# Kernel optimization log

Hardware: AMD Instinct MI355X
Metric: run time of the kernel (lower is better)

## Reference

```python
import jax, jax.numpy as jnp
import numpy as np

EMBED_DIM = 1024
N_HEADS = 16
HEAD_DIM = EMBED_DIM // N_HEADS


def setup_inputs() -> dict:
    key = jax.random.key(0)
    k1, k2, k3 = jax.random.split(key, 3)
    B, T, C = 2, 2048, EMBED_DIM
    x = jax.random.normal(k1, (B, T, C), dtype=jnp.float32)
    # nn.Linear-style init scale
    s = 1.0 / np.sqrt(C)
    Wqkv = jax.random.normal(k2, (C, 3 * C), dtype=jnp.float32) * s
    bqkv = jnp.zeros((3 * C,), dtype=jnp.float32)
    Wout = jax.random.normal(k3, (C, C), dtype=jnp.float32) * s
    bout = jnp.zeros((C,), dtype=jnp.float32)
    return {"x": x, "Wqkv": Wqkv, "bqkv": bqkv, "Wout": Wout, "bout": bout}


def reference(x, Wqkv, bqkv, Wout, bout):
    B, T, C = x.shape
    H, D = N_HEADS, HEAD_DIM
    qkv = x @ Wqkv + bqkv  # [B,T,3C]
    q, k, v = jnp.split(qkv, 3, axis=-1)
    # [B,T,C] -> [B,H,T,D]
    q = q.reshape(B, T, H, D).transpose(0, 2, 1, 3)
    k = k.reshape(B, T, H, D).transpose(0, 2, 1, 3)
    v = v.reshape(B, T, H, D).transpose(0, 2, 1, 3)
    scale = 1.0 / np.sqrt(D)
    scores = jnp.einsum("bhqd,bhkd->bhqk", q, k) * scale  # [B,H,T,T]
    causal = jnp.tril(jnp.ones((T, T), dtype=bool))  # True where allowed
    scores = jnp.where(causal, scores, jnp.finfo(scores.dtype).min)
    attn = jax.nn.softmax(scores, axis=-1)
    out = jnp.einsum("bhqk,bhkd->bhqd", attn, v)  # [B,H,T,D]
    out = out.transpose(0, 2, 1, 3).reshape(B, T, C)
    return out @ Wout + bout
```

## Files before the change

kernel.cpp:

```cpp
#include <hip/hip_runtime.h>
#include <hip/hip_bf16.h>
#include <stdint.h>

#define EMBED 1024
#define NH 16
#define HD 64
#define BATCH 2
#define SEQ 2048
#define MTOK (BATCH*SEQ)

using bf8 = __attribute__((ext_vector_type(8))) short;
using f4  = __attribute__((ext_vector_type(4))) float;
using f16v = __attribute__((ext_vector_type(16))) float;
using u16x4 = __attribute__((ext_vector_type(4))) unsigned short;

union U4 { uint32_t u[4]; bf8 v; };

__device__ __forceinline__ uint32_t pk_bf16(float a, float b) {
  __hip_bfloat162 h = __float22bfloat162_rn(float2{a, b});
  union { __hip_bfloat162 h; uint32_t u; } c; c.h = h; return c.u;
}
__device__ __forceinline__ unsigned short bfbits(float f) {
  __hip_bfloat16 h = __float2bfloat16(f);
  union { __hip_bfloat16 h; unsigned short u; } c; c.h = h; return c.u;
}
__device__ __forceinline__ float bf2f(unsigned short u) {
  union { uint32_t u; float f; } c; c.u = (uint32_t)u << 16; return c.f;
}
__device__ __forceinline__ float fexp2(float x) {
#if __has_builtin(__builtin_amdgcn_exp2f)
  return __builtin_amdgcn_exp2f(x);
#else
  return exp2f(x);
#endif
}
__device__ __forceinline__ float frcp(float x) {
#if __has_builtin(__builtin_amdgcn_rcpf)
  return __builtin_amdgcn_rcpf(x);
#else
  return 1.f / x;
#endif
}

__device__ __forceinline__ void gl2lds16(const void* g, void* l) {
  __builtin_amdgcn_global_load_lds(
      (const __attribute__((address_space(1))) void*)g,
      (__attribute__((address_space(3))) void*)l, 16, 0, 0);
}

__global__ __launch_bounds__(256) void prep(const float* __restrict__ x,
                                            unsigned short* __restrict__ xb,
                                            const float* __restrict__ Wqkv,
                                            unsigned short* __restrict__ wqkvT,
                                            const float* __restrict__ Wout,
                                            unsigned short* __restrict__ woutT) {
  __shared__ float tl[64][65];
  int blk = blockIdx.x;
  if (blk < 4096) {
    int i = (blk * 256 + threadIdx.x) * 4;
    float4 v = *(const float4*)(x + i);
    uint2 o;
    o.x = pk_bf16(v.x, v.y);
    o.y = pk_bf16(v.z, v.w);
    *(uint2*)(xb + i) = o;
    return;
  }
  const float* W; unsigned short* Wt; int K, N, bx, by;
  if (blk < 4096 + 768) {
    int j = blk - 4096; W = Wqkv; Wt = wqkvT; K = 1024; N = 3072;
    bx = j % 48; by = j / 48;
  } else {
    int j = blk - 4096 - 768; W = Wout; Wt = woutT; K = 1024; N = 1024;
    bx = j % 16; by = j / 16;
  }
  int k0 = by * 64, n0 = bx * 64;
  int tr = threadIdx.x >> 6, tc = threadIdx.x & 63;
#pragma unroll
  for (int i = 0; i < 16; i++) {
    int r = tr + i * 4;
    tl[r][tc] = W[(size_t)(k0 + r) * N + n0 + tc];
  }
  __syncthreads();
#pragma unroll
  for (int i = 0; i < 16; i++) {
    int r = tr + i * 4;
    Wt[(size_t)(n0 + r) * K + k0 + tc] = bfbits(tl[tc][r]);
  }
}

template<int MODE>
__global__ __launch_bounds__(256) void gemm_bt(const unsigned short* __restrict__ A,
                                               const unsigned short* __restrict__ Bt,
                                               const float* __restrict__ bias,
                                               unsigned short* __restrict__ Oq,
                                               unsigned short* __restrict__ Ov,
                                               float* __restrict__ Of,
                                               int M, int N, int K) {
  const int tid = threadIdx.x;
  const int w = tid >> 6, lane = tid & 63;
  const int m0 = blockIdx.y * 128, n0 = blockIdx.x * 64;

  __shared__ char smem[49152];
  f4 acc[2][4] = {};

  auto STAGE = [&](int buf, int kk) {
    int k0 = kk * 64;
#pragma unroll
    for (int i = 0; i < 4; i++) {
      int c = i * 4 + w;
      int row = c * 8 + (lane >> 3);
      int col = ((lane & 7) * 8) ^ ((row & 7) << 3);
      gl2lds16(A + (size_t)(m0 + row) * K + k0 + col, smem + buf * 16384 + c * 1024);
    }
#pragma unroll
    for (int i = 0; i < 2; i++) {
      int c = i * 4 + w;
      int row = c * 8 + (lane >> 3);
      int col = ((lane & 7) * 8) ^ ((row & 7) << 3);
      gl2lds16(Bt + (size_t)(n0 + row) * K + k0 + col, smem + 32768 + buf * 8192 + c * 1024);
    }
  };

  const int nk = K / 64;
  STAGE(0, 0);
  STAGE(1, 1);

  for (int kk = 0; kk < nk; kk++) {
    if (kk + 1 < nk) {
      asm volatile("s_waitcnt vmcnt(6)" ::: "memory");
    } else {
      asm volatile("s_waitcnt vmcnt(0)" ::: "memory");
    }
    __builtin_amdgcn_s_barrier();

    const char* Al = smem + (kk & 1) * 16384;
    const char* Bl = smem + 32768 + (kk & 1) * 8192;
    __builtin_amdgcn_s_setprio(1);
#pragma unroll
    for (int ks = 0; ks < 2; ks++) {
      bf8 af[2], bfr[4];
#pragma unroll
      for (int mt = 0; mt < 2; mt++) {
        int rr = w * 32 + mt * 16 + (lane & 15);
        af[mt] = *(const bf8*)(Al + rr * 128 + ((ks * 64 + (lane >> 4) * 16) ^ ((rr & 7) << 4)));
      }
#pragma unroll
      for (int nt = 0; nt < 4; nt++) {
        int rr = nt * 16 + (lane & 15);
        bfr[nt] = *(const bf8*)(Bl + rr * 128 + ((ks * 64 + (lane >> 4) * 16) ^ ((rr & 7) << 4)));
      }
#pragma unroll
      for (int mt = 0; mt < 2; mt++)
#pragma unroll
        for (int nt = 0; nt < 4; nt++)
          acc[mt][nt] = __builtin_amdgcn_mfma_f32_16x16x32_bf16(af[mt], bfr[nt], acc[mt][nt], 0, 0, 0);
    }
    __builtin_amdgcn_s_setprio(0);

    __builtin_amdgcn_s_barrier();
    if (kk + 2 < nk) STAGE(kk & 1, kk + 2);
  }

  if (MODE == 0) {
    const int region = n0 >> 10;
    if (region < 2) {
      float sc = (region == 0) ? 0.180336880f : 1.0f;
#pragma unroll
      for (int nt = 0; nt < 4; nt++) {
        int n = n0 + nt * 16 + (lane & 15);
        float bv = bias[n];
        int c = n & 1023, h = c >> 6, d = c & 63;
#pragma unroll
        for (int mt = 0; mt < 2; mt++) {
#pragma unroll
          for (int r = 0; r < 4; r++) {
            int m = m0 + w * 32 + mt * 16 + (lane >> 4) * 4 + r;
            int b = m >> 11, t = m & 2047;
            size_t off = ((((size_t)region * 2 + b) * 16 + h) * 2048 + t) * 64 + d;
            Oq[off] = bfbits((acc[mt][nt][r] + bv) * sc);
          }
        }
      }
    } else {
#pragma unroll
      for (int nt = 0; nt < 4; nt++) {
        int n = n0 + nt * 16 + (lane & 15);
        float bv = bias[n];
        int c = n & 1023, h = c >> 6, d = c & 63;
#pragma unroll
        for (int mt = 0; mt < 2; mt++) {
          int m = m0 + w * 32 + mt * 16 + (lane >> 4) * 4;
          int b = m >> 11, t = m & 2047;
          size_t off = (((size_t)b * 16 + h) * 64 + d) * 2048 + t;
          u16x4 pk4;
#pragma unroll
          for (int r = 0; r < 4; r++) pk4[r] = bfbits(acc[mt][nt][r] + bv);
          *(u16x4*)(Ov + off) = pk4;
        }
      }
    }
  } else {
#pragma unroll
    for (int mt = 0; mt < 2; mt++) {
#pragma unroll
      for (int r = 0; r < 4; r++) {
        int m = m0 + w * 32 + mt * 16 + (lane >> 4) * 4 + r;
#pragma unroll
        for (int nt = 0; nt < 4; nt++) {
          int n = n0 + nt * 16 + (lane & 15);
          Of[(size_t)m * N + n] = acc[mt][nt][r] + bias[n];
        }
      }
    }
  }
}

__global__ __launch_bounds__(256) void attn12(const unsigned short* __restrict__ Qb,
                                              const unsigned short* __restrict__ Kb,
                                              const unsigned short* __restrict__ Vtb,
                                              unsigned short* __restrict__ Ob,
                                              unsigned short* __restrict__ partO,
                                              float* __restrict__ Lbuf) {
  static const signed char QTs[32] = {15,15,14,14,13,13,12,12,11,11,10,10,9,8,7,6,5,15,4,9,14,3,8,13,2,7,12,1,6,11,0,5};
  static const signed char TSs[32] = {0,11,0,11,0,11,0,11,0,11,0,11,0,0,0,0,0,22,0,11,22,0,11,22,0,11,22,0,11,22,0,11};
  static const signed char PS[32]  = {0,1,2,3,4,5,6,7,8,9,10,11,12,13,14,15,16,17,-1,18,19,-1,20,21,-1,22,23,-1,24,25,-1,26};
  const int idx = blockIdx.x;
  const int s = idx >> 5, bh = idx & 31;
  const int qt = QTs[s], ts = TSs[s];
  const int ntot = 2 * qt + 2;
  const int te = min(ts + 11, ntot);
  const int slot = PS[s];

  const int tid = threadIdx.x;
  const int w = tid >> 6, lane = tid & 63;
  const int hi = lane >> 5, q32 = lane & 31;

  __shared__ char smem[49152];

  const unsigned short* Qg  = Qb  + (size_t)bh * SEQ * HD;
  const unsigned short* Kg  = Kb  + (size_t)bh * SEQ * HD;
  const unsigned short* Vtg = Vtb + (size_t)bh * SEQ * HD;

  const int qbw  = qt * 128 + w * 32;
  const int qrow = qbw + q32;

  bf8 qf[4];
#pragma unroll
  for (int kc = 0; kc < 4; kc++)
    qf[kc] = *(const bf8*)(Qg + (size_t)qrow * HD + kc * 16 + hi * 8);

  f16v acc0 = {}, acc1 = {};
  float lr = 0.f;

  auto STAGE = [&](int buf, int t) {
    int kv0 = t * 64;
#pragma unroll
    for (int i = 0; i < 2; i++) {
      int c = i * 4 + w;
      int row = c * 8 + (lane >> 3);
      int col = ((lane & 7) * 8) ^ ((row & 7) << 3);
      gl2lds16(Kg + (size_t)(kv0 + row) * HD + col,    smem + buf * 8192 + c * 1024);
      gl2lds16(Vtg + (size_t)row * SEQ + kv0 + col,    smem + 24576 + buf * 8192 + c * 1024);
    }
  };

  const int nt_loc = te - ts;
  STAGE(0, ts);
  if (nt_loc > 1) STAGE(1, ts + 1);

  for (int tl = 0; tl < nt_loc; tl++) {
    const int t = ts + tl;
    const int kv0 = t * 64;

    if (tl + 1 < nt_loc) {
      asm volatile("s_waitcnt vmcnt(4)" ::: "memory");
    } else {
      asm volatile("s_waitcnt vmcnt(0)" ::: "memory");
    }
    __builtin_amdgcn_s_barrier();
    if (tl + 2 < nt_loc) STAGE((tl + 2) % 3, t + 2);

    if (kv0 <= qbw + 31) {
      const char* kl = smem + (tl % 3) * 8192;
      const char* vl = smem + 24576 + (tl % 3) * 8192;
      const bool hi_vis = (kv0 + 32 <= qbw + 31);

      f16v s0 = {}, s1 = {};
      __builtin_amdgcn_s_setprio(1);
#pragma unroll
      for (int kc = 0; kc < 4; kc++) {
        int r0 = q32;
        bf8 k0 = *(const bf8*)(kl + r0 * 128 + ((kc * 32 + hi * 16) ^ ((r0 & 7) << 4)));
        s0 = __builtin_amdgcn_mfma_f32_32x32x16_bf16(k0, qf[kc], s0, 0, 0, 0);
      }
      if (hi_vis) {
#pragma unroll
        for (int kc = 0; kc < 4; kc++) {
          int r1 = 32 + q32;
          bf8 k1 = *(const bf8*)(kl + r1 * 128 + ((kc * 32 + hi * 16) ^ ((r1 & 7) << 4)));
          s1 = __builtin_amdgcn_mfma_f32_32x32x16_bf16(k1, qf[kc], s1, 0, 0, 0);
        }
      }
      __builtin_amdgcn_s_setprio(0);

      if (kv0 + 63 > qbw) {
#pragma unroll
        for (int r = 0; r < 16; r++) {
          int key = kv0 + (r & 3) + 8 * (r >> 2) + 4 * hi;
          if (key > qrow)      s0[r] = -1e30f;
          if (key + 32 > qrow) s1[r] = -1e30f;
        }
      }

      uint32_t u[16];
#pragma unroll
      for (int m8 = 0; m8 < 8; m8++) {
        float pa = fexp2(s0[2 * m8]), pb = fexp2(s0[2 * m8 + 1]);
        lr += pa + pb;
        u[m8] = pk_bf16(pa, pb);
      }
      if (hi_vis) {
#pragma unroll
        for (int m8 = 0; m8 < 8; m8++) {
          float pc = fexp2(s1[2 * m8]), pd = fexp2(s1[2 * m8 + 1]);
          lr += pc + pd;
          u[8 + m8] = pk_bf16(pc, pd);
        }
      }

      __builtin_amdgcn_s_setprio(1);
      const int ncc = hi_vis ? 4 : 2;
      for (int kcc = 0; kcc < ncc; kcc++) {
        const int base = (kcc >> 1) * 8 + (kcc & 1) * 4;
        uint32_t a0 = u[base + 0], a2 = u[base + 2];
        uint32_t a1 = u[base + 1], a3 = u[base + 3];
        asm("v_permlane32_swap_b32 %0, %1" : "+v"(a0), "+v"(a2));
        asm("v_permlane32_swap_b32 %0, %1" : "+v"(a1), "+v"(a3));
        U4 f; f.u[0] = a0; f.u[1] = a1; f.u[2] = a2; f.u[3] = a3;
        int r0 = q32, r1 = 32 + q32;
        bf8 v0 = *(const bf8*)(vl + r0 * 128 + ((kcc * 32 + hi * 16) ^ ((r0 & 7) << 4)));
        bf8 v1 = *(const bf8*)(vl + r1 * 128 + ((kcc * 32 + hi * 16) ^ ((r1 & 7) << 4)));
        acc0 = __builtin_amdgcn_mfma_f32_32x32x16_bf16(f.v, v0, acc0, 0, 0, 0);
        acc1 = __builtin_amdgcn_mfma_f32_32x32x16_bf16(f.v, v1, acc1, 0, 0, 0);
      }
      __builtin_amdgcn_s_setprio(0);
    }
  }

  lr += __shfl_xor(lr, 32);
  if (slot < 0) {
    int b = bh >> 4, h = bh & 15;
    unsigned short* Og = Ob + (size_t)b * SEQ * EMBED;
#pragma unroll
    for (int r = 0; r < 16; r++) {
      int ql_ = (r & 3) + 8 * (r >> 2) + 4 * hi;
      float linv = frcp(__shfl(lr, ql_));
      size_t rowoff = (size_t)(qbw + ql_) * EMBED + h * 64;
      Og[rowoff + q32]      = bfbits(acc0[r] * linv);
      Og[rowoff + 32 + q32] = bfbits(acc1[r] * linv);
    }
  } else {
    int pidx = slot * 32 + bh;
    unsigned short* P0 = partO + (size_t)pidx * 8192;
#pragma unroll
    for (int r = 0; r < 16; r++) {
      int ql_ = (r & 3) + 8 * (r >> 2) + 4 * hi;
      int rowl = w * 32 + ql_;
      P0[rowl * 64 + q32]      = bfbits(acc0[r]);
      P0[rowl * 64 + 32 + q32] = bfbits(acc1[r]);
    }
    if (hi == 0) Lbuf[pidx * 128 + w * 32 + q32] = lr;
  }
}

__global__ __launch_bounds__(256) void attn_combine(const unsigned short* __restrict__ partO,
                                                    const float* __restrict__ Lbuf,
                                                    unsigned short* __restrict__ Ob) {
  static const signed char NSg[11] = {2,2,2,2,2,2,3,3,3,3,3};
  static const signed char SL[11][3] = {
    {16,26,0},{15,24,0},{14,22,0},{13,20,0},{12,18,0},{10,11,0},
    {8,9,25},{6,7,23},{4,5,21},{2,3,19},{0,1,17}};
  int pair = blockIdx.x;
  int qi = pair >> 5, bh = pair & 31;
  int qt = 5 + qi;
  int ns = NSg[qi];
  int b = bh >> 4, h = bh & 15;
#pragma unroll
  for (int rr = 0; rr < 2; rr++) {
    int row = rr * 64 + (threadIdx.x >> 2);
    int d0 = (threadIdx.x & 3) * 16;
    float lsum = 0.f;
    float acc[16] = {};
    for (int sg = 0; sg < ns; sg++) {
      int pidx = (int)SL[qi][sg] * 32 + bh;
      lsum += Lbuf[pidx * 128 + row];
      const unsigned short* O0 = partO + (size_t)pidx * 8192 + row * 64 + d0;
#pragma unroll
      for (int v = 0; v < 4; v++) {
        u16x4 a = *(const u16x4*)(O0 + v * 4);
#pragma unroll
        for (int e = 0; e < 4; e++) acc[v * 4 + e] += bf2f(a[e]);
      }
    }
    float linv = 1.f / lsum;
    unsigned short* out = Ob + ((size_t)b * SEQ + qt * 128 + row) * EMBED + h * 64 + d0;
    u16x4 res[4];
#pragma unroll
    for (int v = 0; v < 4; v++) {
#pragma unroll
      for (int e = 0; e < 4; e++) res[v][e] = bfbits(acc[v * 4 + e] * linv);
    }
    *(u16x4*)(out)      = res[0];
    *(u16x4*)(out + 4)  = res[1];
    *(u16x4*)(out + 8)  = res[2];
    *(u16x4*)(out + 12) = res[3];
  }
}

extern "C" void kernel_launch(void* const* d_in, const int* in_sizes, int n_in,
                              void* d_out, int out_size, void* d_ws, size_t ws_size,
                              hipStream_t stream) {
  const float* x    = (const float*)d_in[0];
  const float* Wqkv = (const float*)d_in[1];
  const float* bqkv = (const float*)d_in[2];
  const float* Wout = (const float*)d_in[3];
  const float* bout = (const float*)d_in[4];
  float* out = (float*)d_out;

  char* ws = (char*)d_ws;
  unsigned short* xb    = (unsigned short*)ws;
  unsigned short* wqkvT = (unsigned short*)(ws + (size_t)8 * 1048576);
  unsigned short* partO = (unsigned short*)ws;
  float*          lbuf  = (float*)(ws + 14155776);
  unsigned short* woutT = (unsigned short*)(ws + (size_t)14 * 1048576);
  unsigned short* qk    = (unsigned short*)(ws + (size_t)16 * 1048576);
  unsigned short* vT    = (unsigned short*)(ws + (size_t)32 * 1048576);
  unsigned short* obuf  = (unsigned short*)(ws + (size_t)40 * 1048576);

  prep<<<dim3(4096 + 768 + 256), 256, 0, stream>>>(x, xb, Wqkv, wqkvT, Wout, woutT);

  gemm_bt<0><<<dim3(48, 32), 256, 0, stream>>>(xb, wqkvT, bqkv, qk, vT, nullptr,
                                               MTOK, 3 * EMBED, EMBED);

  const unsigned short* Qb = qk;
  const unsigned short* Kb = qk + (size_t)BATCH * NH * SEQ * HD;
  attn12<<<dim3(32 * 32), 256, 0, stream>>>(Qb, Kb, vT, obuf, partO, lbuf);
  attn_combine<<<dim3(11 * 32), 256, 0, stream>>>(partO, lbuf, obuf);

  gemm_bt<1><<<dim3(16, 32), 256, 0, stream>>>(obuf, woutT, bout, nullptr, nullptr, out,
                                               MTOK, EMBED, EMBED);
}
```

Before: 108.1 us.

## Software-pipeline QK^T of next tile with softmax and PV of current tile

```diff
diff --git a/kernel.cpp b/kernel.cpp
--- a/kernel.cpp
+++ b/kernel.cpp
@@ -215,7 +215,7 @@
   }
 }
 
-__global__ __launch_bounds__(256) void attn12(const unsigned short* __restrict__ Qb,
+__global__ __launch_bounds__(256) void attn13(const unsigned short* __restrict__ Qb,
                                               const unsigned short* __restrict__ Kb,
                                               const unsigned short* __restrict__ Vtb,
                                               unsigned short* __restrict__ Ob,
@@ -264,72 +264,83 @@
     }
   };
 
+  auto QK = [&](const char* kl, bool hv, int kv0, f16v& so0, f16v& so1) {
+    so0 = {}; so1 = {};
+    __builtin_amdgcn_s_setprio(1);
+#pragma unroll
+    for (int kc = 0; kc < 4; kc++) {
+      int r0 = q32;
+      bf8 k0 = *(const bf8*)(kl + r0 * 128 + ((kc * 32 + hi * 16) ^ ((r0 & 7) << 4)));
+      so0 = __builtin_amdgcn_mfma_f32_32x32x16_bf16(k0, qf[kc], so0, 0, 0, 0);
+    }
+    if (hv) {
+#pragma unroll
+      for (int kc = 0; kc < 4; kc++) {
+        int r1 = 32 + q32;
+        bf8 k1 = *(const bf8*)(kl + r1 * 128 + ((kc * 32 + hi * 16) ^ ((r1 & 7) << 4)));
+        so1 = __builtin_amdgcn_mfma_f32_32x32x16_bf16(k1, qf[kc], so1, 0, 0, 0);
+      }
+    }
+    __builtin_amdgcn_s_setprio(0);
+    if (kv0 + 63 > qbw) {
+#pragma unroll
+      for (int r = 0; r < 16; r++) {
+        int key = kv0 + (r & 3) + 8 * (r >> 2) + 4 * hi;
+        if (key > qrow)      so0[r] = -1e30f;
+        if (key + 32 > qrow) so1[r] = -1e30f;
+      }
+    }
+  };
+
   const int nt_loc = te - ts;
+  const int vmaxi = min(nt_loc - 1, (qbw + 31) / 64 - ts);
+
   STAGE(0, ts);
   if (nt_loc > 1) STAGE(1, ts + 1);
+  if (nt_loc > 1) { asm volatile("s_waitcnt vmcnt(4)" ::: "memory"); }
+  else            { asm volatile("s_waitcnt vmcnt(0)" ::: "memory"); }
+  __builtin_amdgcn_s_barrier();
+
+  f16v s0c = {}, s1c = {};
+  bool curv = (vmaxi >= 0);
+  if (curv) QK(smem, (ts * 64 + 32 <= qbw + 31), ts * 64, s0c, s1c);
 
   for (int tl = 0; tl < nt_loc; tl++) {
     const int t = ts + tl;
-    const int kv0 = t * 64;
-
-    if (tl + 1 < nt_loc) {
-      asm volatile("s_waitcnt vmcnt(4)" ::: "memory");
-    } else {
-      asm volatile("s_waitcnt vmcnt(0)" ::: "memory");
-    }
-    __builtin_amdgcn_s_barrier();
-    if (tl + 2 < nt_loc) STAGE((tl + 2) % 3, t + 2);
-
-    if (kv0 <= qbw + 31) {
-      const char* kl = smem + (tl % 3) * 8192;
-      const char* vl = smem + 24576 + (tl % 3) * 8192;
-      const bool hi_vis = (kv0 + 32 <= qbw + 31);
-
-      f16v s0 = {}, s1 = {};
-      __builtin_amdgcn_s_setprio(1);
-#pragma unroll
-      for (int kc = 0; kc < 4; kc++) {
-        int r0 = q32;
-        bf8 k0 = *(const bf8*)(kl + r0 * 128 + ((kc * 32 + hi * 16) ^ ((r0 & 7) << 4)));
-        s0 = __builtin_amdgcn_mfma_f32_32x32x16_bf16(k0, qf[kc], s0, 0, 0, 0);
-      }
-      if (hi_vis) {
-#pragma unroll
-        for (int kc = 0; kc < 4; kc++) {
-          int r1 = 32 + q32;
-          bf8 k1 = *(const bf8*)(kl + r1 * 128 + ((kc * 32 + hi * 16) ^ ((r1 & 7) << 4)));
-          s1 = __builtin_amdgcn_mfma_f32_32x32x16_bf16(k1, qf[kc], s1, 0, 0, 0);
-        }
-      }
-      __builtin_amdgcn_s_setprio(0);
-
-      if (kv0 + 63 > qbw) {
-#pragma unroll
-        for (int r = 0; r < 16; r++) {
-          int key = kv0 + (r & 3) + 8 * (r >> 2) + 4 * hi;
-          if (key > qrow)      s0[r] = -1e30f;
-          if (key + 32 > qrow) s1[r] = -1e30f;
-        }
-      }
-
-      uint32_t u[16];
+    const bool hv = (t * 64 + 32 <= qbw + 31);
+
+    uint32_t u[16];
+    if (curv) {
 #pragma unroll
       for (int m8 = 0; m8 < 8; m8++) {
-        float pa = fexp2(s0[2 * m8]), pb = fexp2(s0[2 * m8 + 1]);
+        float pa = fexp2(s0c[2 * m8]), pb = fexp2(s0c[2 * m8 + 1]);
         lr += pa + pb;
         u[m8] = pk_bf16(pa, pb);
       }
-      if (hi_vis) {
+      if (hv) {
 #pragma unroll
         for (int m8 = 0; m8 < 8; m8++) {
-          float pc = fexp2(s1[2 * m8]), pd = fexp2(s1[2 * m8 + 1]);
+          float pc = fexp2(s1c[2 * m8]), pd = fexp2(s1c[2 * m8 + 1]);
           lr += pc + pd;
           u[8 + m8] = pk_bf16(pc, pd);
         }
       }
-
+    }
+
+    f16v s0n = {}, s1n = {};
+    const bool nextv = (tl + 1 <= vmaxi);
+    if (tl + 1 < nt_loc) {
+      asm volatile("s_waitcnt vmcnt(0)" ::: "memory");
+      __builtin_amdgcn_s_barrier();
+      if (tl + 2 < nt_loc) STAGE((tl + 2) % 3, t + 2);
+      if (nextv)
+        QK(smem + ((tl + 1) % 3) * 8192, ((t + 1) * 64 + 32 <= qbw + 31), (t + 1) * 64, s0n, s1n);
+    }
+
+    if (curv) {
+      const char* vl = smem + 24576 + (tl % 3) * 8192;
       __builtin_amdgcn_s_setprio(1);
-      const int ncc = hi_vis ? 4 : 2;
+      const int ncc = hv ? 4 : 2;
       for (int kcc = 0; kcc < ncc; kcc++) {
         const int base = (kcc >> 1) * 8 + (kcc & 1) * 4;
         uint32_t a0 = u[base + 0], a2 = u[base + 2];
@@ -345,6 +356,8 @@
       }
       __builtin_amdgcn_s_setprio(0);
     }
+
+    s0c = s0n; s1c = s1n; curv = nextv;
   }
 
   lr += __shfl_xor(lr, 32);
@@ -444,7 +457,7 @@
 
   const unsigned short* Qb = qk;
   const unsigned short* Kb = qk + (size_t)BATCH * NH * SEQ * HD;
-  attn12<<<dim3(32 * 32), 256, 0, stream>>>(Qb, Kb, vT, obuf, partO, lbuf);
+  attn13<<<dim3(32 * 32), 256, 0, stream>>>(Qb, Kb, vT, obuf, partO, lbuf);
   attn_combine<<<dim3(11 * 32), 256, 0, stream>>>(partO, lbuf, obuf);
 
   gemm_bt<1><<<dim3(16, 32), 256, 0, stream>>>(obuf, woutT, bout, nullptr, nullptr, out,
```

After: 109.1 us. About the same (+1.0%).
